# Kernel optimization log

Measured on AMD Instinct MI355X. Metric: run time of the kernel, lower is better.

The kernel has to match this reference:

```python
import jax, jax.numpy as jnp
import numpy as np

B, L, S, T, C = 8192, 16, 256, 1000, 500  # trees, leaves/tree, hidden, tables, columns
EPS = 1e-5  # torch LayerNorm default eps


def layer_norm(x, g, b):
    mu = x.mean(-1, keepdims=True)
    var = ((x - mu) ** 2).mean(-1, keepdims=True)
    return (x - mu) * jax.lax.rsqrt(var + EPS) * g + b


def setup_inputs() -> dict:
    key = jax.random.key(0)
    ks = jax.random.split(key, 16)
    s5 = 5 * S

    def lin(k, fan_in, shape):
        bound = 1.0 / np.sqrt(fan_in)
        return jax.random.uniform(k, shape, jnp.float32, -bound, bound)

    return {
        "leaf_ids": jax.random.randint(ks[0], (B, L), 0, T),
        "action_ids": jax.random.randint(ks[1], (B,), 0, T),
        # multi-hot join-condition vectors (original scatters 1s by column index)
        "join_cols": (jax.random.uniform(ks[2], (B, L - 1, C)) < 0.01).astype(jnp.float32),
        "emb": jax.random.normal(ks[3], (T, S), jnp.float32),
        "ln_g": jnp.ones((S,), jnp.float32),
        "ln_b": jnp.zeros((S,), jnp.float32),
        "jc_W": lin(ks[4], C, (C, S)), "jc_b": lin(ks[5], C, (S,)),
        "W1": lin(ks[6], S, (S, s5)), "b1": lin(ks[7], S, (s5,)),
        "W2": lin(ks[8], S, (S, s5)), "b2": lin(ks[9], S, (s5,)),
        "W0": lin(ks[10], S, (S, s5)), "b0": lin(ks[11], S, (s5,)),
        "fc_W": lin(ks[12], 2 * S, (2 * S, S)), "fc_b": lin(ks[13], 2 * S, (S,)),
        "out_W": lin(ks[14], S, (S, 1)), "out_b": lin(ks[15], S, (1,)),
    }


def reference(leaf_ids, action_ids, join_cols, emb, ln_g, ln_b, jc_W, jc_b,
              W1, b1, W2, b2, W0, b0, fc_W, fc_b, out_W, out_b):
    # Leaves: h = LayerNorm(embedding(table_id)), c = 0
    h = layer_norm(emb[leaf_ids], ln_g, ln_b)        # [B, L, S]
    c = jnp.zeros_like(h)
    # Bottom-up level sweep over complete binary trees (log2(L) = 4 levels)
    off, n = 0, L // 2
    while n >= 1:
        hl, hr = h[:, 0::2], h[:, 1::2]               # [B, n, S]
        cl, cr = c[:, 0::2], c[:, 1::2]
        inputx = join_cols[:, off:off + n] @ jc_W + jc_b
        z = hl @ W1 + b1 + hr @ W2 + b2 + inputx @ W0 + b0  # [B, n, 5S]
        a, i, f1, f2, o = jnp.split(z, 5, axis=-1)
        c = jnp.tanh(a) * jax.nn.sigmoid(i) + jax.nn.sigmoid(f1) * cl + jax.nn.sigmoid(f2) * cr
        h = jax.nn.sigmoid(o) * jnp.tanh(c)
        off += n
        n //= 2
    state_h = h[:, 0]                                 # [B, S] root encodings
    action_h = layer_norm(emb[action_ids], ln_g, ln_b)  # [B, S] action leaf encodings
    x = jnp.concatenate([state_h, action_h], axis=-1)   # [B, 2S]
    return jax.nn.relu(x @ fc_W + fc_b) @ out_W + out_b  # [B, 1]
```

## Files before the change

### kernel.cpp

```cpp
#include <hip/hip_runtime.h>
#include <hip/hip_bf16.h>
#include <stdint.h>

#define NB 8192
#define NL 16
#define NS 256
#define NT 1000
#define NC 500
#define NS5 1280
#define NROWS_JC (NB*15)

typedef __attribute__((ext_vector_type(8))) short bf16x8;
typedef __attribute__((ext_vector_type(4))) float f32x4;

typedef __attribute__((address_space(1))) const void gas_void;
typedef __attribute__((address_space(3))) void las_void;

__device__ __forceinline__ void g2l16(const void* g, void* l) {
  __builtin_amdgcn_global_load_lds((gas_void*)g, (las_void*)l, 16, 0, 0);
}

__device__ __forceinline__ float sigf(float x) { return 1.f / (1.f + __expf(-x)); }
__device__ __forceinline__ float tanhfast(float x) {
  float e = __expf(2.f * fabsf(x));
  float t = 1.f - 2.f / (e + 1.f);
  return copysignf(t, x);
}
__device__ __forceinline__ unsigned short bf16b(float x) {
  __hip_bfloat16 h = __float2bfloat16(x);
  return *reinterpret_cast<unsigned short*>(&h);
}
__device__ __forceinline__ float b2f(unsigned short v) {
  union { unsigned u; float f; } x;
  x.u = (unsigned)v << 16;
  return x.f;
}

__device__ __forceinline__ int origcol(int slice, int nc) {
  int q = nc / 80, rem = nc % 80;
  int g = rem / 16, u16 = rem % 16;
  int U = slice * 64 + q * 16 + u16;
  return g * 256 + U;
}

__global__ __launch_bounds__(256) void ln_kernel(
    const float* __restrict__ emb, const float* __restrict__ g,
    const float* __restrict__ b, unsigned short* __restrict__ ob16) {
  int t = blockIdx.x;
  int i = threadIdx.x;
  int lane = i & 63, wv = i >> 6;
  float x = emb[t * NS + i];
  float s = x, s2 = x * x;
  for (int o = 1; o < 64; o <<= 1) {
    s += __shfl_xor(s, o);
    s2 += __shfl_xor(s2, o);
  }
  __shared__ float rs[4], rs2[4];
  if (lane == 0) { rs[wv] = s; rs2[wv] = s2; }
  __syncthreads();
  float S = rs[0] + rs[1] + rs[2] + rs[3];
  float S2 = rs2[0] + rs2[1] + rs2[2] + rs2[3];
  float mu = S * (1.f / NS);
  float var = S2 * (1.f / NS) - mu * mu;
  float y = (x - mu) * rsqrtf(var + 1e-5f) * g[i] + b[i];
  ob16[t * NS + i] = bf16b(y);
}

__global__ __launch_bounds__(256) void pack_w12(
    const float* __restrict__ W1, const float* __restrict__ W2,
    const float* __restrict__ W0, unsigned short* __restrict__ out) {
  int e = blockIdx.x * 256 + threadIdx.x;
  if (e >= 4 * 24 * 320 * 4) return;
  int kg = e & 3;
  int r = e >> 2;
  int nc = r % 320; r /= 320;
  int kc = r % 24;
  int slice = r / 24;
  int oc = origcol(slice, nc);
  int kbase = kc * 32 + kg * 8;
  unsigned short tmp[8];
#pragma unroll
  for (int j = 0; j < 8; ++j) {
    int k = kbase + j;
    float x;
    if (k < 256) x = W1[(size_t)k * NS5 + oc];
    else if (k < 512) x = W2[(size_t)(k - 256) * NS5 + oc];
    else x = W0[(size_t)(k - 512) * NS5 + oc];
    tmp[j] = bf16b(x);
  }
  ushort4 v0 = make_ushort4(tmp[0], tmp[1], tmp[2], tmp[3]);
  ushort4 v1 = make_ushort4(tmp[4], tmp[5], tmp[6], tmp[7]);
  size_t dst = (size_t)(slice * 24 + kc) * 20480 + (size_t)nc * 64 + kg * 16;
  *(ushort4*)((char*)out + dst) = v0;
  *(ushort4*)((char*)out + dst + 8) = v1;
}

__global__ __launch_bounds__(256) void pack_fcw(
    const float* __restrict__ fcW, unsigned short* __restrict__ out) {
  int e = blockIdx.x * 256 + threadIdx.x;
  if (e >= 16 * 256 * 4) return;
  int kg = e & 3;
  int r = e >> 2;
  int nc = r & 255;
  int kc = r >> 8;
  int kbase = kc * 32 + kg * 8;
  unsigned short tmp[8];
#pragma unroll
  for (int j = 0; j < 8; ++j) tmp[j] = bf16b(fcW[(size_t)(kbase + j) * NS + nc]);
  ushort4 v0 = make_ushort4(tmp[0], tmp[1], tmp[2], tmp[3]);
  ushort4 v1 = make_ushort4(tmp[4], tmp[5], tmp[6], tmp[7]);
  size_t dst = (size_t)kc * 16384 + (size_t)nc * 64 + kg * 16;
  *(ushort4*)((char*)out + dst) = v0;
  *(ushort4*)((char*)out + dst + 8) = v1;
}

__global__ __launch_bounds__(256) void bias_kernel(
    const float* __restrict__ b1, const float* __restrict__ b2,
    const float* __restrict__ b0, float* __restrict__ bias_zp) {
  int pc = blockIdx.x * 256 + threadIdx.x;
  if (pc >= NS5) return;
  int slice = pc / 320, nc = pc % 320;
  int oc = origcol(slice, nc);
  bias_zp[pc] = b1[oc] + b2[oc] + b0[oc];
}

__global__ __launch_bounds__(256) void inputx_kernel(
    const float* __restrict__ jc, const float* __restrict__ jcW,
    const float* __restrict__ jcb, unsigned short* __restrict__ outp) {
  int wv = threadIdx.x >> 6, lane = threadIdx.x & 63;
  size_t row0 = (size_t)blockIdx.x * 8 + wv * 2;
  const float* jr0 = jc + row0 * NC;
  const float* jr1 = jc + (row0 + 1) * NC;
  float4 p0 = *(const float4*)(jr0 + lane * 4);
  float4 q0 = *(const float4*)(jr1 + lane * 4);
  float4 p1 = make_float4(0.f, 0.f, 0.f, 0.f);
  float4 q1 = make_float4(0.f, 0.f, 0.f, 0.f);
  if (lane < 61) {
    p1 = *(const float4*)(jr0 + 256 + lane * 4);
    q1 = *(const float4*)(jr1 + 256 + lane * 4);
  }
  const float4 jb = *(const float4*)(jcb + lane * 4);
  float a0 = jb.x, a1 = jb.y, a2 = jb.z, a3 = jb.w;
  float b0 = jb.x, b1 = jb.y, b2 = jb.z, b3 = jb.w;

#define GATHER_MASK(val, cbase, d0, d1, d2, d3)                       \
  {                                                                   \
    unsigned long long m = __ballot((val) != 0.f);                    \
    while (m) {                                                       \
      int l = __ffsll(m) - 1;                                         \
      m &= m - 1;                                                     \
      int c = (cbase) + l * 4;                                        \
      const float4 w = *(const float4*)(jcW + (size_t)c * NS + lane * 4); \
      d0 += w.x; d1 += w.y; d2 += w.z; d3 += w.w;                     \
    }                                                                 \
  }
  GATHER_MASK(p0.x, 0, a0, a1, a2, a3) GATHER_MASK(p0.y, 1, a0, a1, a2, a3)
  GATHER_MASK(p0.z, 2, a0, a1, a2, a3) GATHER_MASK(p0.w, 3, a0, a1, a2, a3)
  GATHER_MASK(p1.x, 256, a0, a1, a2, a3) GATHER_MASK(p1.y, 257, a0, a1, a2, a3)
  GATHER_MASK(p1.z, 258, a0, a1, a2, a3) GATHER_MASK(p1.w, 259, a0, a1, a2, a3)
  GATHER_MASK(q0.x, 0, b0, b1, b2, b3) GATHER_MASK(q0.y, 1, b0, b1, b2, b3)
  GATHER_MASK(q0.z, 2, b0, b1, b2, b3) GATHER_MASK(q0.w, 3, b0, b1, b2, b3)
  GATHER_MASK(q1.x, 256, b0, b1, b2, b3) GATHER_MASK(q1.y, 257, b0, b1, b2, b3)
  GATHER_MASK(q1.z, 258, b0, b1, b2, b3) GATHER_MASK(q1.w, 259, b0, b1, b2, b3)
#undef GATHER_MASK

  ushort4 o;
  o.x = bf16b(a0); o.y = bf16b(a1); o.z = bf16b(a2); o.w = bf16b(a3);
  *(ushort4*)(outp + row0 * NS + lane * 4) = o;
  o.x = bf16b(b0); o.y = bf16b(b1); o.z = bf16b(b2); o.w = bf16b(b3);
  *(ushort4*)(outp + (row0 + 1) * NS + lane * 4) = o;
}

template <bool FIRST, bool LAST>
__global__ __launch_bounds__(256, 2) void level_kernel(
    const unsigned short* __restrict__ h_in,
    const unsigned* __restrict__ c_in,
    const unsigned short* __restrict__ inpx,
    const unsigned short* __restrict__ w12p,
    const float* __restrict__ bias_zp,
    unsigned short* __restrict__ h_out,
    unsigned* __restrict__ c_out,
    unsigned short* __restrict__ state_out,
    const int* __restrict__ leaf,
    int log2n, int joff) {
  __shared__ __align__(1024) char ldsA[2 * 16384];
  const int tid = threadIdx.x, lane = tid & 63, wv = tid >> 6;
  const int m0 = blockIdx.x * 128;
  const int slice = blockIdx.y;
  const int n = 1 << log2n;

  f32x4 acc[8][5];
#pragma unroll
  for (int a = 0; a < 8; ++a)
#pragma unroll
    for (int t = 0; t < 5; ++t) acc[a][t] = (f32x4){0.f, 0.f, 0.f, 0.f};

  const int rl64 = wv * 16 + (lane >> 2);
  const int ss = (lane & 3) ^ ((rl64 >> 1) & 3);
  const int mlo = m0 + rl64, mhi = mlo + 64;
  const char* h0lo; const char* h1lo; const char* h0hi; const char* h1hi;
  if (FIRST) {
    h0lo = (const char*)h_in + ((size_t)leaf[2 * mlo] * 512 + (size_t)ss * 16);
    h1lo = (const char*)h_in + ((size_t)leaf[2 * mlo + 1] * 512 + (size_t)ss * 16);
    h0hi = (const char*)h_in + ((size_t)leaf[2 * mhi] * 512 + (size_t)ss * 16);
    h1hi = (const char*)h_in + ((size_t)leaf[2 * mhi + 1] * 512 + (size_t)ss * 16);
  } else {
    h0lo = (const char*)h_in + ((size_t)mlo * 1024 + (size_t)ss * 16);
    h1lo = h0lo;
    h0hi = (const char*)h_in + ((size_t)mhi * 1024 + (size_t)ss * 16);
    h1hi = h0hi;
  }
  const char* xlo = (const char*)inpx +
      (((size_t)(mlo >> log2n) * 15 + joff + (mlo & (n - 1))) * 512 + (size_t)ss * 16);
  const char* xhi = (const char*)inpx +
      (((size_t)(mhi >> log2n) * 15 + joff + (mhi & (n - 1))) * 512 + (size_t)ss * 16);
  char* adst = ldsA + wv * 1024;

  auto srcA = [&](int kc, int j) -> const char* {
    const char* h0 = j ? h0hi : h0lo;
    const char* h1 = j ? h1hi : h1lo;
    const char* xs = j ? xhi : xlo;
    if (FIRST) {
      return (kc < 8) ? h0 + kc * 64
           : (kc < 16) ? h1 + (kc - 8) * 64
                       : xs + (kc - 16) * 64;
    }
    return (kc < 16) ? h0 + kc * 64 : xs + (kc - 16) * 64;
  };
  auto stageA = [&](int kt, int buf) {
    char* db = adst + buf * 16384;
    g2l16(srcA(2 * kt, 0), db);
    g2l16(srcA(2 * kt, 1), db + 4096);
    g2l16(srcA(2 * kt + 1, 0), db + 8192);
    g2l16(srcA(2 * kt + 1, 1), db + 12288);
  };

  const int aoff = (lane & 15) * 64 + (((lane >> 4) ^ ((lane >> 1) & 3)) << 4);
  const char* gB = (const char*)w12p + (size_t)slice * 24 * 20480 +
                   (size_t)(wv * 80 + (lane & 15)) * 64 + (size_t)(lane >> 4) * 16;

  bf16x8 bcur[5], bnxt[5];
  auto loadB = [&](int kc, bf16x8* dst) {
    const char* gk = gB + (size_t)kc * 20480;
#pragma unroll
    for (int g = 0; g < 5; ++g) dst[g] = *(const bf16x8*)(gk + g * 1024);
  };

#define CLUSTER(pA, bset)                                                           \
  {                                                                                 \
    bf16x8 a0 = *(const bf16x8*)(pA);                                               \
    bf16x8 a1 = *(const bf16x8*)((pA) + 1024);                                      \
    bf16x8 a2 = *(const bf16x8*)((pA) + 2048);                                      \
    bf16x8 a3 = *(const bf16x8*)((pA) + 3072);                                      \
    bf16x8 a4 = *(const bf16x8*)((pA) + 4096);                                      \
    bf16x8 a5 = *(const bf16x8*)((pA) + 5120);                                      \
    bf16x8 a6 = *(const bf16x8*)((pA) + 6144);                                      \
    bf16x8 a7 = *(const bf16x8*)((pA) + 7168);                                      \
    _Pragma("unroll")                                                               \
    for (int g = 0; g < 5; ++g) {                                                   \
      acc[0][g] = __builtin_amdgcn_mfma_f32_16x16x32_bf16(a0, bset[g], acc[0][g], 0, 0, 0); \
      acc[1][g] = __builtin_amdgcn_mfma_f32_16x16x32_bf16(a1, bset[g], acc[1][g], 0, 0, 0); \
      acc[2][g] = __builtin_amdgcn_mfma_f32_16x16x32_bf16(a2, bset[g], acc[2][g], 0, 0, 0); \
      acc[3][g] = __builtin_amdgcn_mfma_f32_16x16x32_bf16(a3, bset[g], acc[3][g], 0, 0, 0); \
      acc[4][g] = __builtin_amdgcn_mfma_f32_16x16x32_bf16(a4, bset[g], acc[4][g], 0, 0, 0); \
      acc[5][g] = __builtin_amdgcn_mfma_f32_16x16x32_bf16(a5, bset[g], acc[5][g], 0, 0, 0); \
      acc[6][g] = __builtin_amdgcn_mfma_f32_16x16x32_bf16(a6, bset[g], acc[6][g], 0, 0, 0); \
      acc[7][g] = __builtin_amdgcn_mfma_f32_16x16x32_bf16(a7, bset[g], acc[7][g], 0, 0, 0); \
    }                                                                               \
  }

  stageA(0, 0);
  loadB(0, bcur);
  asm volatile("s_waitcnt vmcnt(0)" ::: "memory");
  __builtin_amdgcn_s_barrier();

  for (int kt = 0; kt < 12; ++kt) {
    const int buf = kt & 1;
    stageA(kt < 11 ? kt + 1 : 11, buf ^ 1);
    __builtin_amdgcn_sched_barrier(0);
    loadB(2 * kt + 1, bnxt);
    const char* pA = ldsA + buf * 16384 + aoff;
    CLUSTER(pA, bcur);
    loadB(2 * kt + 2 < 24 ? 2 * kt + 2 : 0, bcur);
    CLUSTER(pA + 8192, bnxt);
    __builtin_amdgcn_sched_barrier(0);
    asm volatile("s_waitcnt vmcnt(5)" ::: "memory");
    __builtin_amdgcn_sched_barrier(0);
    __builtin_amdgcn_s_barrier();
  }
#undef CLUSTER

  float bias[5];
#pragma unroll
  for (int g = 0; g < 5; ++g)
    bias[g] = bias_zp[slice * 320 + wv * 80 + g * 16 + (lane & 15)];
  const int u = slice * 64 + wv * 16 + (lane & 15);

#pragma unroll
  for (int rt = 0; rt < 8; ++rt) {
    const int base = m0 + rt * 16 + (lane >> 4) * 4;
    float hv[4], cv[4];
#pragma unroll
    for (int r = 0; r < 4; ++r) {
      int row = base + r;
      float za = acc[rt][0][r] + bias[0];
      float zi = acc[rt][1][r] + bias[1];
      float zo = acc[rt][4][r] + bias[4];
      float cnew = tanhfast(za) * sigf(zi);
      if (!FIRST) {
        float zf1 = acc[rt][2][r] + bias[2];
        float zf2 = acc[rt][3][r] + bias[3];
        unsigned pc = c_in[(size_t)row * NS + u];
        float cl = b2f((unsigned short)(pc & 0xffff));
        float cr = b2f((unsigned short)(pc >> 16));
        cnew += sigf(zf1) * cl + sigf(zf2) * cr;
      }
      cv[r] = cnew;
      hv[r] = sigf(zo) * tanhfast(cnew);
    }
    if (LAST) {
#pragma unroll
      for (int r = 0; r < 4; ++r)
        state_out[(size_t)(base + r) * NS + u] = bf16b(hv[r]);
    } else {
#pragma unroll
      for (int r = 0; r < 4; ++r)
        h_out[(size_t)(base + r) * NS + u] = bf16b(hv[r]);
      const size_t pb = (size_t)(base >> 1) * NS + u;
      c_out[pb] = (unsigned)bf16b(cv[0]) | ((unsigned)bf16b(cv[1]) << 16);
      c_out[pb + NS] = (unsigned)bf16b(cv[2]) | ((unsigned)bf16b(cv[3]) << 16);
    }
  }
}

__global__ __launch_bounds__(256, 2) void fc_mfma(
    const unsigned short* __restrict__ stateb,
    const unsigned short* __restrict__ ln_b16,
    const int* __restrict__ action_ids, const unsigned short* __restrict__ fcwp,
    const float* __restrict__ fcb, const float* __restrict__ outW,
    const float* __restrict__ outb, float* __restrict__ out) {
  __shared__ __align__(1024) char ldsA[2 * 8192];
  __shared__ float red[64][4];
  const int tid = threadIdx.x, lane = tid & 63, wv = tid >> 6;
  const int m0 = blockIdx.x * 64;

  f32x4 acc[4][4];
#pragma unroll
  for (int a = 0; a < 4; ++a)
#pragma unroll
    for (int t = 0; t < 4; ++t) acc[a][t] = (f32x4){0.f, 0.f, 0.f, 0.f};

  const int rl = wv * 16 + (lane >> 2);
  const int ss = (lane & 3) ^ ((rl >> 1) & 3);
  const int m = m0 + rl;
  const char* src0 = (const char*)stateb + ((size_t)m * 512 + (size_t)ss * 16);
  const char* src1 =
      (const char*)ln_b16 + ((size_t)action_ids[m] * 512 + (size_t)ss * 16);
  char* adst = ldsA + wv * 1024;

  auto srcA = [&](int kc) -> const char* {
    return (kc < 8) ? src0 + kc * 64 : src1 + (kc - 8) * 64;
  };
  auto stageA = [&](int kt, int buf) {
    g2l16(srcA(2 * kt), adst + buf * 8192);
    g2l16(srcA(2 * kt + 1), adst + buf * 8192 + 4096);
  };

  const int aoff = (lane & 15) * 64 + (((lane >> 4) ^ ((lane >> 1) & 3)) << 4);
  const char* gB = (const char*)fcwp +
                   (size_t)(wv * 64 + (lane & 15)) * 64 + (size_t)(lane >> 4) * 16;

  bf16x8 bcur[4], bnxt[4];
  auto loadB = [&](int kc, bf16x8* dst) {
    const char* gk = gB + (size_t)kc * 16384;
#pragma unroll
    for (int t = 0; t < 4; ++t) dst[t] = *(const bf16x8*)(gk + t * 1024);
  };

  stageA(0, 0);
  loadB(0, bcur);
  asm volatile("s_waitcnt vmcnt(0)" ::: "memory");
  __builtin_amdgcn_s_barrier();

  for (int kt = 0; kt < 8; ++kt) {
    const int buf = kt & 1;
    stageA(kt < 7 ? kt + 1 : 7, buf ^ 1);
    __builtin_amdgcn_sched_barrier(0);
    loadB(2 * kt + 1, bnxt);
    const char* pA = ldsA + buf * 8192 + aoff;
    bf16x8 a0 = *(const bf16x8*)(pA);
    bf16x8 a1 = *(const bf16x8*)(pA + 1024);
    bf16x8 a2 = *(const bf16x8*)(pA + 2048);
    bf16x8 a3 = *(const bf16x8*)(pA + 3072);
#pragma unroll
    for (int t = 0; t < 4; ++t) {
      acc[0][t] = __builtin_amdgcn_mfma_f32_16x16x32_bf16(a0, bcur[t], acc[0][t], 0, 0, 0);
      acc[1][t] = __builtin_amdgcn_mfma_f32_16x16x32_bf16(a1, bcur[t], acc[1][t], 0, 0, 0);
      acc[2][t] = __builtin_amdgcn_mfma_f32_16x16x32_bf16(a2, bcur[t], acc[2][t], 0, 0, 0);
      acc[3][t] = __builtin_amdgcn_mfma_f32_16x16x32_bf16(a3, bcur[t], acc[3][t], 0, 0, 0);
    }
    loadB(2 * kt + 2 < 16 ? 2 * kt + 2 : 0, bcur);
    bf16x8 c0 = *(const bf16x8*)(pA + 4096);
    bf16x8 c1 = *(const bf16x8*)(pA + 5120);
    bf16x8 c2 = *(const bf16x8*)(pA + 6144);
    bf16x8 c3 = *(const bf16x8*)(pA + 7168);
#pragma unroll
    for (int t = 0; t < 4; ++t) {
      acc[0][t] = __builtin_amdgcn_mfma_f32_16x16x32_bf16(c0, bnxt[t], acc[0][t], 0, 0, 0);
      acc[1][t] = __builtin_amdgcn_mfma_f32_16x16x32_bf16(c1, bnxt[t], acc[1][t], 0, 0, 0);
      acc[2][t] = __builtin_amdgcn_mfma_f32_16x16x32_bf16(c2, bnxt[t], acc[2][t], 0, 0, 0);
      acc[3][t] = __builtin_amdgcn_mfma_f32_16x16x32_bf16(c3, bnxt[t], acc[3][t], 0, 0, 0);
    }
    __builtin_amdgcn_sched_barrier(0);
    asm volatile("s_waitcnt vmcnt(4)" ::: "memory");
    __builtin_amdgcn_sched_barrier(0);
    __builtin_amdgcn_s_barrier();
  }

  float fb[4], ow[4];
#pragma unroll
  for (int t = 0; t < 4; ++t) {
    int col = wv * 64 + t * 16 + (lane & 15);
    fb[t] = fcb[col];
    ow[t] = outW[col];
  }
#pragma unroll
  for (int rt = 0; rt < 4; ++rt) {
#pragma unroll
    for (int r = 0; r < 4; ++r) {
      float s = 0.f;
#pragma unroll
      for (int t = 0; t < 4; ++t)
        s += fmaxf(acc[rt][t][r] + fb[t], 0.f) * ow[t];
      s += __shfl_xor(s, 1);
      s += __shfl_xor(s, 2);
      s += __shfl_xor(s, 4);
      s += __shfl_xor(s, 8);
      if ((lane & 15) == 0) red[rt * 16 + (lane >> 4) * 4 + r][wv] = s;
    }
  }
  __syncthreads();
  if (tid < 64)
    out[m0 + tid] = red[tid][0] + red[tid][1] + red[tid][2] + red[tid][3] + outb[0];
}

extern "C" void kernel_launch(void* const* d_in, const int* in_sizes, int n_in,
                              void* d_out, int out_size, void* d_ws, size_t ws_size,
                              hipStream_t stream) {
  const int* leaf_ids = (const int*)d_in[0];
  const int* action_ids = (const int*)d_in[1];
  const float* join_cols = (const float*)d_in[2];
  const float* emb = (const float*)d_in[3];
  const float* ln_g = (const float*)d_in[4];
  const float* ln_b = (const float*)d_in[5];
  const float* jc_W = (const float*)d_in[6];
  const float* jc_b = (const float*)d_in[7];
  const float* W1 = (const float*)d_in[8];
  const float* b1 = (const float*)d_in[9];
  const float* W2 = (const float*)d_in[10];
  const float* b2 = (const float*)d_in[11];
  const float* W0 = (const float*)d_in[12];
  const float* b0 = (const float*)d_in[13];
  const float* fc_W = (const float*)d_in[14];
  const float* fc_b = (const float*)d_in[15];
  const float* out_W = (const float*)d_in[16];
  const float* out_b = (const float*)d_in[17];

  char* ws = (char*)d_ws;
  size_t o = 0;
  auto alloc = [&](size_t bytes) {
    size_t r = o;
    o += (bytes + 255) & ~(size_t)255;
    return r;
  };
  unsigned short* ln_b16 = (unsigned short*)(ws + alloc((size_t)NT * NS * 2));
  unsigned short* w12p = (unsigned short*)(ws + alloc((size_t)4 * 24 * 20480));
  unsigned short* fcwp = (unsigned short*)(ws + alloc((size_t)16 * 16384));
  float* bias_zp = (float*)(ws + alloc((size_t)NS5 * 4));
  unsigned short* inpx = (unsigned short*)(ws + alloc((size_t)NROWS_JC * NS * 2));
  unsigned short* hX = (unsigned short*)(ws + alloc((size_t)NB * 8 * NS * 2));
  unsigned short* hY = (unsigned short*)(ws + alloc((size_t)NB * 4 * NS * 2));
  unsigned* cX = (unsigned*)(ws + alloc((size_t)NB * 8 * NS * 2));
  unsigned* cY = (unsigned*)(ws + alloc((size_t)NB * 4 * NS * 2));
  unsigned short* stateb = (unsigned short*)(ws + alloc((size_t)NB * NS * 2));
  (void)ws_size; (void)in_sizes; (void)n_in; (void)out_size;

  ln_kernel<<<NT, 256, 0, stream>>>(emb, ln_g, ln_b, ln_b16);
  pack_w12<<<480, 256, 0, stream>>>(W1, W2, W0, w12p);
  pack_fcw<<<64, 256, 0, stream>>>(fc_W, fcwp);
  bias_kernel<<<5, 256, 0, stream>>>(b1, b2, b0, bias_zp);
  inputx_kernel<<<NROWS_JC / 8, 256, 0, stream>>>(join_cols, jc_W, jc_b, inpx);

  level_kernel<true, false><<<dim3(512, 4), 256, 0, stream>>>(
      ln_b16, nullptr, inpx, w12p, bias_zp, hX, cX, nullptr, leaf_ids, 3, 0);
  level_kernel<false, false><<<dim3(256, 4), 256, 0, stream>>>(
      hX, cX, inpx, w12p, bias_zp, hY, cY, nullptr, leaf_ids, 2, 8);
  level_kernel<false, false><<<dim3(128, 4), 256, 0, stream>>>(
      hY, cY, inpx, w12p, bias_zp, hX, cX, nullptr, leaf_ids, 1, 12);
  level_kernel<false, true><<<dim3(64, 4), 256, 0, stream>>>(
      hX, cX, inpx, w12p, bias_zp, nullptr, nullptr, stateb, leaf_ids, 0, 14);

  fc_mfma<<<NB / 64, 256, 0, stream>>>(stateb, ln_b16, action_ids, fcwp, fc_b,
                                       out_W, out_b, (float*)d_out);
}
```

Baseline: 355.3 us.

## Deepen A-tile staging to four k-chunks per barrier and pair jc gathers

The level kernel now stages four k-chunks of A per pipeline step into a doubled LDS buffer (64KB), halving the number of main-loop iterations and block-wide barriers while rotating B register loads across four MFMA clusters. The join-column gather loop processes two set bits per iteration to issue two independent weight loads at once. Doubling LDS per block may reduce occupancy below the 2-blocks target, and the waitcnt(5) now covers more outstanding loads.

```diff
diff --git a/kernel.cpp b/kernel.cpp
--- a/kernel.cpp
+++ b/kernel.cpp
@@ -143,16 +143,22 @@
   float a0 = jb.x, a1 = jb.y, a2 = jb.z, a3 = jb.w;
   float b0 = jb.x, b1 = jb.y, b2 = jb.z, b3 = jb.w;
 
-#define GATHER_MASK(val, cbase, d0, d1, d2, d3)                       \
-  {                                                                   \
-    unsigned long long m = __ballot((val) != 0.f);                    \
-    while (m) {                                                       \
-      int l = __ffsll(m) - 1;                                         \
-      m &= m - 1;                                                     \
-      int c = (cbase) + l * 4;                                        \
-      const float4 w = *(const float4*)(jcW + (size_t)c * NS + lane * 4); \
-      d0 += w.x; d1 += w.y; d2 += w.z; d3 += w.w;                     \
-    }                                                                 \
+#define GATHER_MASK(val, cbase, d0, d1, d2, d3)                               \
+  {                                                                           \
+    unsigned long long m = __ballot((val) != 0.f);                            \
+    while (m) {                                                               \
+      int l0 = __ffsll(m) - 1; m &= m - 1;                                    \
+      bool has1 = (m != 0ULL);                                                \
+      int l1 = has1 ? __ffsll(m) - 1 : l0;                                    \
+      if (has1) m &= m - 1;                                                   \
+      const float4 w0 =                                                       \
+          *(const float4*)(jcW + (size_t)((cbase) + l0 * 4) * NS + lane * 4); \
+      const float4 w1 =                                                       \
+          *(const float4*)(jcW + (size_t)((cbase) + l1 * 4) * NS + lane * 4); \
+      float f1 = has1 ? 1.f : 0.f;                                            \
+      d0 += w0.x + f1 * w1.x; d1 += w0.y + f1 * w1.y;                         \
+      d2 += w0.z + f1 * w1.z; d3 += w0.w + f1 * w1.w;                         \
+    }                                                                         \
   }
   GATHER_MASK(p0.x, 0, a0, a1, a2, a3) GATHER_MASK(p0.y, 1, a0, a1, a2, a3)
   GATHER_MASK(p0.z, 2, a0, a1, a2, a3) GATHER_MASK(p0.w, 3, a0, a1, a2, a3)
@@ -183,7 +189,7 @@
     unsigned short* __restrict__ state_out,
     const int* __restrict__ leaf,
     int log2n, int joff) {
-  __shared__ __align__(1024) char ldsA[2 * 16384];
+  __shared__ __align__(1024) char ldsA[2 * 32768];
   const int tid = threadIdx.x, lane = tid & 63, wv = tid >> 6;
   const int m0 = blockIdx.x * 128;
   const int slice = blockIdx.y;
@@ -227,19 +233,20 @@
     }
     return (kc < 16) ? h0 + kc * 64 : xs + (kc - 16) * 64;
   };
-  auto stageA = [&](int kt, int buf) {
-    char* db = adst + buf * 16384;
-    g2l16(srcA(2 * kt, 0), db);
-    g2l16(srcA(2 * kt, 1), db + 4096);
-    g2l16(srcA(2 * kt + 1, 0), db + 8192);
-    g2l16(srcA(2 * kt + 1, 1), db + 12288);
+  auto stageA4 = [&](int kt, int buf) {
+    char* db = adst + buf * 32768;
+#pragma unroll
+    for (int j = 0; j < 4; ++j) {
+      g2l16(srcA(4 * kt + j, 0), db + j * 8192);
+      g2l16(srcA(4 * kt + j, 1), db + j * 8192 + 4096);
+    }
   };
 
   const int aoff = (lane & 15) * 64 + (((lane >> 4) ^ ((lane >> 1) & 3)) << 4);
   const char* gB = (const char*)w12p + (size_t)slice * 24 * 20480 +
                    (size_t)(wv * 80 + (lane & 15)) * 64 + (size_t)(lane >> 4) * 16;
 
-  bf16x8 bcur[5], bnxt[5];
+  bf16x8 bA[5], bB[5];
   auto loadB = [&](int kc, bf16x8* dst) {
     const char* gk = gB + (size_t)kc * 20480;
 #pragma unroll
@@ -269,20 +276,24 @@
     }                                                                               \
   }
 
-  stageA(0, 0);
-  loadB(0, bcur);
+  stageA4(0, 0);
+  loadB(0, bA);
   asm volatile("s_waitcnt vmcnt(0)" ::: "memory");
   __builtin_amdgcn_s_barrier();
 
-  for (int kt = 0; kt < 12; ++kt) {
+  for (int kt = 0; kt < 6; ++kt) {
     const int buf = kt & 1;
-    stageA(kt < 11 ? kt + 1 : 11, buf ^ 1);
+    stageA4(kt < 5 ? kt + 1 : 5, buf ^ 1);
     __builtin_amdgcn_sched_barrier(0);
-    loadB(2 * kt + 1, bnxt);
-    const char* pA = ldsA + buf * 16384 + aoff;
-    CLUSTER(pA, bcur);
-    loadB(2 * kt + 2 < 24 ? 2 * kt + 2 : 0, bcur);
-    CLUSTER(pA + 8192, bnxt);
+    loadB(4 * kt + 1, bB);
+    const char* pA = ldsA + buf * 32768 + aoff;
+    CLUSTER(pA, bA);
+    loadB(4 * kt + 2, bA);
+    CLUSTER(pA + 8192, bB);
+    loadB(4 * kt + 3, bB);
+    CLUSTER(pA + 16384, bA);
+    loadB((4 * kt + 4) < 24 ? 4 * kt + 4 : 0, bA);
+    CLUSTER(pA + 24576, bB);
     __builtin_amdgcn_sched_barrier(0);
     asm volatile("s_waitcnt vmcnt(5)" ::: "memory");
     __builtin_amdgcn_sched_barrier(0);
```

Measured after the change: 376.7 us. 6.0% more time.
